# Kernel tuning notes

Measured on AMD Instinct MI355X. Metric: run time of the kernel, lower is better.

The kernel has to match this reference:

```python
import jax, jax.numpy as jnp
import numpy as np

EPS = 1e-12

def _l2norm(v, axis):
    return v / jnp.maximum(jnp.linalg.norm(v, axis=axis, keepdims=True), EPS)

def setup_inputs() -> dict:
    key = jax.random.key(0)
    k1, k2, k3 = jax.random.split(key, 3)
    B, D, C = 65536, 768, 100
    P = C * (C - 1) // 2  # 4950 pairwise local heads
    x = jax.random.normal(k1, (B, D), dtype=jnp.float32)
    first_out = jax.random.normal(k2, (B, C), dtype=jnp.float32)
    weights = jax.random.normal(k3, (P, 2, D), dtype=jnp.float32) * (1.0 / np.sqrt(D))
    sigma = jnp.ones((P,), dtype=jnp.float32)
    return {"x": x, "first_out": first_out, "weights": weights, "sigma": sigma, "cur_stage": 4}

def reference(x, first_out, weights, sigma, cur_stage):
    # top-2 class indices per sample, sorted ascending -> pair key (a, b), a < b
    _, top2 = jax.lax.top_k(first_out, 2)              # [B, 2]
    sorted_idx = jnp.sort(top2, axis=1)                # [B, 2]
    a = sorted_idx[:, 0]
    b = sorted_idx[:, 1]
    pair_idx = b * (b - 1) // 2 + a                    # key 'a-b' -> flat head index
    W = weights[pair_idx]                              # [B, 2, D] gathered expert weights
    s = sigma[pair_idx]                                # [B]
    # CosineLinear (use_RP=False): sigma * normalize(x) @ normalize(W)^T
    xn = _l2norm(x, axis=1)                            # [B, D]
    Wn = _l2norm(W, axis=2)                            # [B, 2, D]
    logits = s[:, None] * jnp.einsum('bd,bkd->bk', xn, Wn)  # [B, 2]
    # pick which of the two candidate classes the local head prefers
    sel = jnp.argmax(logits, axis=1)                   # [B]
    preds = jnp.take_along_axis(sorted_idx, sel[:, None], axis=1)[:, 0]  # [B]
    return preds, logits
```

## Files before the change

kernel.cpp:

```cpp
#include <hip/hip_runtime.h>
#include <math.h>


#define D_DIM 768
#define C_DIM 100
#define EPS_N 1e-12

typedef float vf4 __attribute__((ext_vector_type(4)));

#define ROW_SHR1    0x111
#define ROW_SHR2    0x112
#define ROW_SHR4    0x114
#define ROW_SHR8    0x118
#define ROW_BCAST15 0x142
#define ROW_BCAST31 0x143

template <int CTRL>
__device__ __forceinline__ float dpp0_f32(float v) {
    return __builtin_bit_cast(float, __builtin_amdgcn_update_dpp(
        0, __builtin_bit_cast(int, v), CTRL, 0xF, 0xF, true));
}

template <int CTRL>
__device__ __forceinline__ double dpp0_f64(double v) {
    union { double d; unsigned long long u; } x; x.d = v;
    int lo = (int)(unsigned int)(x.u & 0xffffffffull);
    int hi = (int)(unsigned int)(x.u >> 32);
    int olo = __builtin_amdgcn_update_dpp(0, lo, CTRL, 0xF, 0xF, true);
    int ohi = __builtin_amdgcn_update_dpp(0, hi, CTRL, 0xF, 0xF, true);
    union { unsigned long long u; double d; } y;
    y.u = ((unsigned long long)(unsigned int)ohi << 32) | (unsigned int)olo;
    return y.d;
}

__device__ __forceinline__ float wave_sum_f32(float v) {
    v += dpp0_f32<ROW_SHR1>(v);
    v += dpp0_f32<ROW_SHR2>(v);
    v += dpp0_f32<ROW_SHR4>(v);
    v += dpp0_f32<ROW_SHR8>(v);
    v += dpp0_f32<ROW_BCAST15>(v);
    v += dpp0_f32<ROW_BCAST31>(v);
    return v;
}

__device__ __forceinline__ double wave_sum_f64(double v) {
    v += dpp0_f64<ROW_SHR1>(v);
    v += dpp0_f64<ROW_SHR2>(v);
    v += dpp0_f64<ROW_SHR4>(v);
    v += dpp0_f64<ROW_SHR8>(v);
    v += dpp0_f64<ROW_BCAST15>(v);
    v += dpp0_f64<ROW_BCAST31>(v);
    return v;
}

__device__ __forceinline__ bool vi_gt(float v0, int i0, float v1, int i1) {
    return (v0 > v1) || (v0 == v1 && i0 < i1);
}

template <int CTRL>
__device__ __forceinline__ void t2_step(float& v1, int& i1, float& v2, int& i2) {
    const int NEGINF = 0xFF800000;
    const int BIGIDX = 0x7fffffff;
    float ov1 = __builtin_bit_cast(float, __builtin_amdgcn_update_dpp(
        NEGINF, __builtin_bit_cast(int, v1), CTRL, 0xF, 0xF, false));
    int   oi1 = __builtin_amdgcn_update_dpp(BIGIDX, i1, CTRL, 0xF, 0xF, false);
    float ov2 = __builtin_bit_cast(float, __builtin_amdgcn_update_dpp(
        NEGINF, __builtin_bit_cast(int, v2), CTRL, 0xF, 0xF, false));
    int   oi2 = __builtin_amdgcn_update_dpp(BIGIDX, i2, CTRL, 0xF, 0xF, false);
    if (vi_gt(ov1, oi1, v1, i1)) {
        float nv2; int ni2;
        if (vi_gt(v1, i1, ov2, oi2)) { nv2 = v1;  ni2 = i1; }
        else                         { nv2 = ov2; ni2 = oi2; }
        v1 = ov1; i1 = oi1; v2 = nv2; i2 = ni2;
    } else {
        if (vi_gt(ov1, oi1, v2, i2)) { v2 = ov1; i2 = oi1; }
    }
}

__global__ __launch_bounds__(256) void norm_kernel(
    const float* __restrict__ weights,
    const float* __restrict__ sigma,
    double* __restrict__ q,
    int P2)
{
    const int lane = threadIdx.x & 63;
    const int t = (blockIdx.x << 2) + (threadIdx.x >> 6);
    if (t >= P2) return;

    const vf4* wv = (const vf4*)(weights + (size_t)t * D_DIM);
    vf4 a0 = wv[lane], a1 = wv[lane + 64], a2 = wv[lane + 128];

    double n = 0.0;
#define SQ(a)                                                                  \
    n += (double)a.x * a.x + (double)a.y * a.y                                 \
       + (double)a.z * a.z + (double)a.w * a.w;
    SQ(a0) SQ(a1) SQ(a2)
#undef SQ
    n = wave_sum_f64(n);
    if (lane == 63) {
        q[t] = (double)sigma[t >> 1] / fmax(sqrt(n), EPS_N);
    }
}

__global__ __launch_bounds__(256) void mlcl_kernel(
    const float* __restrict__ x,
    const float* __restrict__ first_out,
    const float* __restrict__ weights,
    const double* __restrict__ q,
    float* __restrict__ out,
    int B)
{
    const int lane = threadIdx.x & 63;
    const int r = (blockIdx.x << 2) + (threadIdx.x >> 6);
    if (r >= B) return;

    const float* fo = first_out + (size_t)r * C_DIM;
    float e0 = fo[lane];
    int   j1 = lane + 64;
    float e1 = (j1 < C_DIM) ? fo[j1] : -INFINITY;

    const vf4* xv = (const vf4*)(x + (size_t)r * D_DIM);
    vf4 xa0 = xv[lane], xa1 = xv[lane + 64], xa2 = xv[lane + 128];

    float v1, v2; int i1, i2;
    if (vi_gt(e1, j1, e0, lane)) { v1 = e1; i1 = j1;   v2 = e0; i2 = lane; }
    else                         { v1 = e0; i1 = lane; v2 = e1; i2 = j1; }

    t2_step<ROW_SHR1>(v1, i1, v2, i2);
    t2_step<ROW_SHR2>(v1, i1, v2, i2);
    t2_step<ROW_SHR4>(v1, i1, v2, i2);
    t2_step<ROW_SHR8>(v1, i1, v2, i2);
    t2_step<ROW_BCAST15>(v1, i1, v2, i2);
    t2_step<ROW_BCAST31>(v1, i1, v2, i2);
    const int gi1 = __builtin_amdgcn_readlane(i1, 63);
    const int gi2 = __builtin_amdgcn_readlane(i2, 63);
    const int a = min(gi1, gi2);
    const int b = max(gi1, gi2);
    const int p = b * (b - 1) / 2 + a;

    const double q0 = q[2 * (size_t)p];
    const double q1 = q[2 * (size_t)p + 1];

    const vf4* wv = (const vf4*)(weights + (size_t)p * (2 * D_DIM));
    vf4 w00 = wv[lane],       w01 = wv[lane + 64],       w02 = wv[lane + 128];
    vf4 w10 = wv[192 + lane], w11 = wv[192 + lane + 64], w12 = wv[192 + lane + 128];

    float  xx = 0.f;
    double d0 = 0.0, d1 = 0.0;
#define ACC(xa, w0, w1)                                                       \
    xx += xa.x * xa.x + xa.y * xa.y + xa.z * xa.z + xa.w * xa.w;              \
    d0 += (double)xa.x * w0.x + (double)xa.y * w0.y                           \
        + (double)xa.z * w0.z + (double)xa.w * w0.w;                          \
    d1 += (double)xa.x * w1.x + (double)xa.y * w1.y                           \
        + (double)xa.z * w1.z + (double)xa.w * w1.w;
    ACC(xa0, w00, w10)
    ACC(xa1, w01, w11)
    ACC(xa2, w02, w12)
#undef ACC

    xx = wave_sum_f32(xx);
    d0 = wave_sum_f64(d0);
    d1 = wave_sum_f64(d1);

    if (lane == 63) {
        const double inx = 1.0 / fmax(sqrt((double)xx), EPS_N);
        const double l0  = q0 * d0 * inx;
        const double l1  = q1 * d1 * inx;
        const int sel = (l1 > l0) ? 1 : 0;
        out[r] = (float)(sel ? b : a);
        float2 lg = make_float2((float)l0, (float)l1);
        *(float2*)(out + B + 2 * (size_t)r) = lg;
    }
}

extern "C" void kernel_launch(void* const* d_in, const int* in_sizes, int n_in,
                              void* d_out, int out_size, void* d_ws, size_t ws_size,
                              hipStream_t stream) {
    const float* x         = (const float*)d_in[0];
    const float* first_out = (const float*)d_in[1];
    const float* weights   = (const float*)d_in[2];
    const float* sigma     = (const float*)d_in[3];
    float* out = (float*)d_out;
    double* q  = (double*)d_ws;

    const int B  = in_sizes[0] / D_DIM;
    const int P2 = in_sizes[2] / D_DIM;

    hipLaunchKernelGGL(norm_kernel, dim3((P2 + 3) / 4), dim3(256), 0, stream,
                       weights, sigma, q, P2);
    hipLaunchKernelGGL(mlcl_kernel, dim3((B + 3) / 4), dim3(256), 0, stream,
                       x, first_out, weights, q, out, B);
}
```

Before: 321.4 us.

## Bucket rows by expert pair via histogram, scan and scatter before dot products

Splits the fused kernel into top-2 plus histogram, a single-block prefix scan, a scatter that builds a permutation, and a main kernel that processes rows grouped by pair index. Rows that share an expert pair run in adjacent waves, so they hit the same weight rows in cache instead of gathering randomly across 4950 heads. In exchange it adds three extra launches, atomics, a serial one-block scan, and an indirect, non-coalesced read of x through the permutation.

Result: slower. 346.2 us (+7.7%).

```diff
diff --git a/kernel.cpp b/kernel.cpp
--- a/kernel.cpp
+++ b/kernel.cpp
@@ -81,8 +81,12 @@
     const float* __restrict__ weights,
     const float* __restrict__ sigma,
     double* __restrict__ q,
-    int P2)
-{
+    unsigned* __restrict__ hist,
+    int P2, int nbins)
+{
+    const int gid = blockIdx.x * 256 + threadIdx.x;
+    if (gid < nbins) hist[gid] = 0u;
+
     const int lane = threadIdx.x & 63;
     const int t = (blockIdx.x << 2) + (threadIdx.x >> 6);
     if (t >= P2) return;
@@ -102,12 +106,10 @@
     }
 }
 
-__global__ __launch_bounds__(256) void mlcl_kernel(
-    const float* __restrict__ x,
+__global__ __launch_bounds__(256) void topk_hist_kernel(
     const float* __restrict__ first_out,
-    const float* __restrict__ weights,
-    const double* __restrict__ q,
-    float* __restrict__ out,
+    unsigned* __restrict__ pb,
+    unsigned* __restrict__ hist,
     int B)
 {
     const int lane = threadIdx.x & 63;
@@ -118,9 +120,6 @@
     float e0 = fo[lane];
     int   j1 = lane + 64;
     float e1 = (j1 < C_DIM) ? fo[j1] : -INFINITY;
-
-    const vf4* xv = (const vf4*)(x + (size_t)r * D_DIM);
-    vf4 xa0 = xv[lane], xa1 = xv[lane + 64], xa2 = xv[lane + 128];
 
     float v1, v2; int i1, i2;
     if (vi_gt(e1, j1, e0, lane)) { v1 = e1; i1 = j1;   v2 = e0; i2 = lane; }
@@ -132,14 +131,89 @@
     t2_step<ROW_SHR8>(v1, i1, v2, i2);
     t2_step<ROW_BCAST15>(v1, i1, v2, i2);
     t2_step<ROW_BCAST31>(v1, i1, v2, i2);
-    const int gi1 = __builtin_amdgcn_readlane(i1, 63);
-    const int gi2 = __builtin_amdgcn_readlane(i2, 63);
-    const int a = min(gi1, gi2);
-    const int b = max(gi1, gi2);
+
+    if (lane == 63) {
+        const int a = min(i1, i2);
+        const int b = max(i1, i2);
+        const int p = b * (b - 1) / 2 + a;
+        pb[r] = ((unsigned)a << 17) | ((unsigned)b << 24);
+        atomicAdd(&hist[p], 1u);
+    }
+}
+
+#define SCAN_T 1024
+#define BINS_PER_T 5
+__global__ __launch_bounds__(SCAN_T) void scan_kernel(
+    const unsigned* __restrict__ hist,
+    unsigned* __restrict__ ofs,
+    int nbins)
+{
+    __shared__ unsigned lds[SCAN_T];
+    const int t = threadIdx.x;
+    unsigned loc[BINS_PER_T];
+    unsigned s = 0;
+#pragma unroll
+    for (int k = 0; k < BINS_PER_T; ++k) {
+        int idx = t * BINS_PER_T + k;
+        unsigned v = (idx < nbins) ? hist[idx] : 0u;
+        loc[k] = s;
+        s += v;
+    }
+    lds[t] = s;
+    __syncthreads();
+    for (int d = 1; d < SCAN_T; d <<= 1) {
+        unsigned v = (t >= d) ? lds[t - d] : 0u;
+        __syncthreads();
+        lds[t] += v;
+        __syncthreads();
+    }
+    unsigned base = (t > 0) ? lds[t - 1] : 0u;
+#pragma unroll
+    for (int k = 0; k < BINS_PER_T; ++k) {
+        int idx = t * BINS_PER_T + k;
+        if (idx < nbins) ofs[idx] = base + loc[k];
+    }
+}
+
+__global__ __launch_bounds__(256) void scatter_kernel(
+    const unsigned* __restrict__ pb,
+    unsigned* __restrict__ ofs,
+    unsigned* __restrict__ perm,
+    int B)
+{
+    const int r = blockIdx.x * 256 + threadIdx.x;
+    if (r >= B) return;
+    const unsigned v = pb[r];
+    const int a = (int)((v >> 17) & 0x7f);
+    const int b = (int)((v >> 24) & 0x7f);
+    const int p = b * (b - 1) / 2 + a;
+    const unsigned slot = atomicAdd(&ofs[p], 1u);
+    perm[slot] = v | (unsigned)r;
+}
+
+__global__ __launch_bounds__(256) void mlcl_main(
+    const float* __restrict__ x,
+    const float* __restrict__ weights,
+    const double* __restrict__ q,
+    const unsigned* __restrict__ perm,
+    float* __restrict__ out,
+    int B)
+{
+    const int lane = threadIdx.x & 63;
+    const int i = (blockIdx.x << 2) + (threadIdx.x >> 6);
+    if (i >= B) return;
+
+    const int e = __builtin_amdgcn_readfirstlane((int)perm[i]);
+    const int r = e & 0x1ffff;
+    const int a = (e >> 17) & 0x7f;
+    const int b = (e >> 24) & 0x7f;
     const int p = b * (b - 1) / 2 + a;
 
     const double q0 = q[2 * (size_t)p];
     const double q1 = q[2 * (size_t)p + 1];
+
+    const vf4* xv = (const vf4*)(x + (size_t)r * D_DIM);
+    vf4 xa0 = xv[lane], xa1 = xv[lane + 64], xa2 = xv[lane + 128];
 
     const vf4* wv = (const vf4*)(weights + (size_t)p * (2 * D_DIM));
     vf4 w00 = wv[lane],       w01 = wv[lane + 64],       w02 = wv[lane + 128];
@@ -181,13 +255,27 @@
     const float* weights   = (const float*)d_in[2];
     const float* sigma     = (const float*)d_in[3];
     float* out = (float*)d_out;
-    double* q  = (double*)d_ws;
 
     const int B  = in_sizes[0] / D_DIM;
     const int P2 = in_sizes[2] / D_DIM;
+    const int NB = P2 / 2;
+
+    char* ws = (char*)d_ws;
+    size_t o = 0;
+    double*   q    = (double*)(ws + o);  o += ((size_t)P2 * 8 + 255) & ~255ull;
+    unsigned* hist = (unsigned*)(ws + o); o += ((size_t)NB * 4 + 255) & ~255ull;
+    unsigned* ofs  = (unsigned*)(ws + o); o += ((size_t)NB * 4 + 255) & ~255ull;
+    unsigned* pb   = (unsigned*)(ws + o); o += ((size_t)B * 4 + 255) & ~255ull;
+    unsigned* perm = (unsigned*)(ws + o);
 
     hipLaunchKernelGGL(norm_kernel, dim3((P2 + 3) / 4), dim3(256), 0, stream,
-                       weights, sigma, q, P2);
-    hipLaunchKernelGGL(mlcl_kernel, dim3((B + 3) / 4), dim3(256), 0, stream,
-                       x, first_out, weights, q, out, B);
-}
+                       weights, sigma, q, hist, P2, NB);
+    hipLaunchKernelGGL(topk_hist_kernel, dim3((B + 3) / 4), dim3(256), 0, stream,
+                       first_out, pb, hist, B);
+    hipLaunchKernelGGL(scan_kernel, dim3(1), dim3(SCAN_T), 0, stream,
+                       hist, ofs, NB);
+    hipLaunchKernelGGL(scatter_kernel, dim3((B + 255) / 256), dim3(256), 0, stream,
+                       pb, ofs, perm, B);
+    hipLaunchKernelGGL(mlcl_main, dim3((B + 3) / 4), dim3(256), 0, stream,
+                       x, weights, q, perm, out, B);
+}
```
